# Performance work log

Measured on AMD Instinct MI355X. Metric: run time of the kernel, lower is better.

Reference implementation:

```python
import jax, jax.numpy as jnp
from jax import lax
import numpy as np

EVAL_TERMS = 10   # eval mode: num_terms = eval_terms, update_iters = 0
INIT_ITERS = 50   # power iterations done in __init__
KSIZE = 3
IDX = np.array([0, 1, 1, 2, 3, 4, 2, 4, 3])  # maps 5 coeffs -> 3x3 kernel
EPS = 1e-12


def _l2n(t, axis):
    return t / (jnp.sqrt(jnp.sum(t * t, axis=axis, keepdims=True)) + EPS)


def setup_inputs() -> dict:
    key = jax.random.key(0)
    kx, kw, kb, ku, kv = jax.random.split(key, 5)
    C = 64
    stdv = 1.0 / np.sqrt(C)
    return {
        "x": jax.random.normal(kx, (16, C, 192, 192), dtype=jnp.float32),
        "random_conv_filter": jax.random.normal(kw, (C, C, 5), dtype=jnp.float32) * stdv,
        "bias": jax.random.uniform(kb, (C,), dtype=jnp.float32, minval=-stdv, maxval=stdv),
        "u0": jax.random.normal(ku, (5, 1, C), dtype=jnp.float32),
        "v0": jax.random.normal(kv, (5, C, 1), dtype=jnp.float32),
    }


def _power_iter(A, u0, v0):
    # A: (num, C, C) (stop-gradient), u: (num,1,C), v: (num,C,1)
    u = _l2n(u0, 2)
    v = _l2n(v0, 1)
    def body(i, uv):
        u, v = uv
        v = _l2n(jnp.sum(A * u, axis=2, keepdims=True), 1)
        u = _l2n(jnp.sum(A * v, axis=1, keepdims=True), 2)
        return (u, v)
    return lax.fori_loop(0, INIT_ITERS, body, (u, v))


def reference(x, random_conv_filter, bias, u0, v0):
    C = random_conv_filter.shape[0]
    # skew-symmetric filter per coefficient slice: A = 0.5*(W - W^T)
    A = 0.5 * (random_conv_filter - jnp.transpose(random_conv_filter, (1, 0, 2)))
    A = jnp.transpose(A, (2, 0, 1))  # (num, C, C)
    # spectral norm via power iteration (buffers; no grad)
    u, v = _power_iter(lax.stop_gradient(A), u0, v0)
    u = lax.stop_gradient(u)
    v = lax.stop_gradient(v)
    sigmas = jnp.sum(A * v * u, axis=(1, 2))  # (num,), grad flows through A only
    An = A / sigmas[:, None, None]
    # Taylor series of expm: I + An + An^2/2! + ... (eval_terms=10)
    curr = An
    Fm = An
    for i in range(2, EVAL_TERMS + 1):
        curr = jnp.einsum('nij,njk->nik', curr, An) / float(i)
        Fm = Fm + curr
    Fm = Fm + jnp.eye(C, dtype=Fm.dtype)[None]
    Fm = jnp.transpose(Fm, (1, 2, 0))  # (C, C, num)
    # expand 5 coeffs to 3x3 kernel, then spatial ifft2 -> real
    K = Fm[:, :, IDX].reshape(C, C, KSIZE, KSIZE)
    K = jnp.fft.ifft2(K, axes=(-2, -1)).real.astype(x.dtype)
    w = x.shape[2]
    pad = w // KSIZE  # circular pad and matching dilation
    xp = jnp.pad(x, ((0, 0), (0, 0), (pad, pad), (pad, pad)), mode='wrap')
    z = lax.conv_general_dilated(
        xp, K, window_strides=(1, 1), padding='VALID',
        rhs_dilation=(pad, pad),
        dimension_numbers=('NCHW', 'OIHW', 'NCHW'))
    return z + bias[None, :, None, None]
```

## Files before the change

kernel.cpp:

```cpp
#include <hip/hip_runtime.h>

typedef __attribute__((ext_vector_type(8))) short short8;
typedef __attribute__((ext_vector_type(4))) float f32x4;
typedef __attribute__((ext_vector_type(4))) float float4v;
typedef __attribute__((ext_vector_type(4))) unsigned int u32x4;

__device__ __forceinline__ unsigned short f2bf(float f) {
    unsigned int u = __float_as_uint(f);
    u += 0x7fffu + ((u >> 16) & 1u);
    return (unsigned short)(u >> 16);
}

__device__ __forceinline__ float wavesum(float x) {
#pragma unroll
    for (int m = 1; m < 64; m <<= 1) x += __shfl_xor(x, m);
    return x;
}

__device__ __forceinline__ float wavemax(float x) {
#pragma unroll
    for (int m = 1; m < 64; m <<= 1) x = fmaxf(x, __shfl_xor(x, m));
    return x;
}

__device__ __forceinline__ float matvec64(const float* row, float y) {
    float ac[8] = {0.f, 0.f, 0.f, 0.f, 0.f, 0.f, 0.f, 0.f};
#pragma unroll
    for (int j = 0; j < 64; ++j) {
        const float yj =
            __uint_as_float(__builtin_amdgcn_readlane(__float_as_uint(y), j));
        ac[j & 7] = fmaf(row[j], yj, ac[j & 7]);
    }
    return ((ac[0] + ac[1]) + (ac[2] + ac[3])) + ((ac[4] + ac[5]) + (ac[6] + ac[7]));
}

__device__ __forceinline__ void gload16(const void* g, void* l) {
    __builtin_amdgcn_global_load_lds(
        (const __attribute__((address_space(1))) unsigned int*)g,
        (__attribute__((address_space(3))) unsigned int*)l, 16, 0, 0);
}

#define WTF_OFF       81920
#define WTOLD_OFF     745472
#define WS_NEEDED     1409024UL

#define FM_AFP   0
#define FM_R0    17408
#define FM_R1    34816
#define FM_SLOT  52224
#define FM_RED   76800
#define FM_SMEM  76928

__device__ __forceinline__ void fm_matmul_sb(char* sm, int srcOff, int bfSrcSlot,
                                             int dstOff, int bfDstSlot, int t) {
    const float* src = (const float*)(sm + srcOff);
    const unsigned short* bfS =
        (const unsigned short*)(sm + FM_SLOT) + bfSrcSlot * 4096;
    float* dst = (float*)(sm + dstOff);
    float* redf = (float*)(sm + FM_RED);
    const int lane = t & 63;
    const int wv = t >> 6;
    const int lm = lane & 15, lg = lane >> 4;
    f32x4 acc[4] = {};
    if (t < 256) {
#pragma unroll
        for (int kk = 0; kk < 2; ++kk) {
            const float* ap = src + (16 * wv + lm) * 68 + kk * 32 + lg * 8;
            const f32x4 a0 = *(const f32x4*)ap;
            const f32x4 a1 = *(const f32x4*)(ap + 4);
            short8 ah;
#pragma unroll
            for (int j = 0; j < 4; ++j) {
                ah[j] = (short)f2bf(a0[j]);
                ah[j + 4] = (short)f2bf(a1[j]);
            }
#pragma unroll
            for (int cf = 0; cf < 4; ++cf) {
                const short8 b =
                    *(const short8*)(bfS + ((kk * 4 + cf) * 64 + lane) * 8);
                acc[cf] = __builtin_amdgcn_mfma_f32_16x16x32_bf16(ah, b, acc[cf],
                                                                  0, 0, 0);
            }
        }
        float mx = 0.0f;
#pragma unroll
        for (int cf = 0; cf < 4; ++cf)
#pragma unroll
            for (int r = 0; r < 4; ++r) mx = fmaxf(mx, fabsf(acc[cf][r]));
        mx = wavemax(mx);
        if (lane == 0) redf[wv] = mx;
    }
    __syncthreads();
    if (t < 256) {
        const float g = fmaxf(fmaxf(redf[0], redf[1]), fmaxf(redf[2], redf[3]));
        const float sc = 1.0f / g;
        unsigned short* bfD = (unsigned short*)(sm + FM_SLOT) + bfDstSlot * 4096;
#pragma unroll
        for (int cf = 0; cf < 4; ++cf) {
#pragma unroll
            for (int r = 0; r < 4; ++r) {
                const int k = 16 * wv + 4 * lg + r;
                const int nn = 16 * cf + lm;
                const float v = acc[cf][r] * sc;
                dst[k * 68 + nn] = v;
                if (bfDstSlot >= 0)
                    bfD[(((k >> 5) * 4 + cf) * 64 + ((k & 31) >> 3) * 16 + lm) * 8 +
                        (k & 7)] = f2bf(v);
            }
        }
    }
    __syncthreads();
}

__global__ __launch_bounds__(512) void fm_kernel(const float* __restrict__ W,
                                                 const float* __restrict__ u0,
                                                 float* __restrict__ FmOut) {
    __shared__ __align__(16) char smem[FM_SMEM];
    const int t = threadIdx.x;
    float* Afp = (float*)(smem + FM_AFP);
    float* R0f = (float*)(smem + FM_R0);
    float* R1f = (float*)(smem + FM_R1);
    float* redf = (float*)(smem + FM_RED);
    float* sigP = redf + 4;
    const int n = blockIdx.x;
    const int lane = t & 63;
    const int wv = t >> 6;
    const int lm = lane & 15, lg = lane >> 4;

    {
        const int i = t >> 3;
        const int j0 = (t & 7) * 8;
#pragma unroll
        for (int k = 0; k < 8; ++k) {
            const int j = j0 + k;
            const float wij = W[(i * 64 + j) * 5 + n];
            const float wji = W[(j * 64 + i) * 5 + n];
            Afp[i * 68 + j] = 0.5f * (wij - wji);
        }
    }
    __syncthreads();

    if (t < 256) {
        unsigned short* s0 = (unsigned short*)(smem + FM_SLOT);
#pragma unroll
        for (int cf = 0; cf < 4; ++cf) {
#pragma unroll
            for (int r = 0; r < 4; ++r) {
                const int k = 16 * wv + 4 * lg + r;
                const int nn = 16 * cf + lm;
                s0[(((k >> 5) * 4 + cf) * 64 + ((k & 31) >> 3) * 16 + lm) * 8 +
                   (k & 7)] = f2bf(Afp[k * 68 + nn]);
            }
        }
    }
    __syncthreads();

    fm_matmul_sb(smem, FM_AFP, 0, FM_R0, 1, t);
    fm_matmul_sb(smem, FM_R0, 1, FM_R1, 2, t);
    fm_matmul_sb(smem, FM_R1, 2, FM_R0, 0, t);
    fm_matmul_sb(smem, FM_R0, 0, FM_R1, 2, t);
    fm_matmul_sb(smem, FM_R1, 2, FM_R0, 0, t);
    fm_matmul_sb(smem, FM_R0, 0, FM_R1, -1, t);
    fm_matmul_sb(smem, FM_R1, 0, FM_R0, -1, t);
    fm_matmul_sb(smem, FM_R0, 1, FM_R1, -1, t);

    if (t < 64) {
        float row[64];
#pragma unroll
        for (int q = 0; q < 16; ++q)
            *(f32x4*)&row[q * 4] = *(const f32x4*)&R1f[t * 68 + q * 4];
        float u = u0[n * 64 + t];
        u = u / (sqrtf(wavesum(u * u)) + 1e-12f);
        const float w = matvec64(row, u);
#pragma unroll
        for (int q = 0; q < 16; ++q)
            *(f32x4*)&row[q * 4] = *(const f32x4*)&Afp[t * 68 + q * 4];
        const float tt = matvec64(row, w);
        const float v = tt / (sqrtf(wavesum(tt * tt)) + 1e-12f);
        const float s = matvec64(row, v);
        const float u50 = -s / (sqrtf(wavesum(s * s)) + 1e-12f);
        const float t2 = matvec64(row, u50);
        const float sig = wavesum(v * t2);
        if (t == 0) *sigP = sig;
    }
    __syncthreads();

    const float inv_sig = 1.0f / (*sigP);
    float Fm[4][4];
    if (t < 256) {
        unsigned int* Anpk = (unsigned int*)(smem + FM_SLOT);
#pragma unroll
        for (int cf = 0; cf < 4; ++cf) {
#pragma unroll
            for (int r = 0; r < 4; ++r) {
                const int k = 16 * wv + 4 * lg + r;
                const int nn = 16 * cf + lm;
                const float v = Afp[k * 68 + nn] * inv_sig;
                R0f[k * 68 + nn] = v;
                const unsigned int ph = f2bf(v);
                const float hf = __uint_as_float(ph << 16);
                const unsigned int pl = f2bf(v - hf);
                Anpk[(((k >> 5) * 4 + cf) * 64 + ((k & 31) >> 3) * 16 + lm) * 8 +
                     (k & 7)] = ph | (pl << 16);
                Fm[cf][r] = v;
            }
        }
    }
    __syncthreads();

    for (int term = 2; term <= 10; ++term) {
        f32x4 acc[4] = {};
        if (t < 256) {
            const unsigned int* Anpk = (const unsigned int*)(smem + FM_SLOT);
#pragma unroll
            for (int kk = 0; kk < 2; ++kk) {
                const float* ap = R0f + (16 * wv + lm) * 68 + kk * 32 + lg * 8;
                const f32x4 a0 = *(const f32x4*)ap;
                const f32x4 a1 = *(const f32x4*)(ap + 4);
                short8 ah, al;
#pragma unroll
                for (int j = 0; j < 4; ++j) {
                    const unsigned int h0 = f2bf(a0[j]);
                    ah[j] = (short)h0;
                    al[j] = (short)f2bf(a0[j] - __uint_as_float(h0 << 16));
                    const unsigned int h1 = f2bf(a1[j]);
                    ah[j + 4] = (short)h1;
                    al[j + 4] = (short)f2bf(a1[j] - __uint_as_float(h1 << 16));
                }
#pragma unroll
                for (int cf = 0; cf < 4; ++cf) {
                    const unsigned int* pp = Anpk + ((kk * 4 + cf) * 64 + lane) * 8;
                    const u32x4 p0 = *(const u32x4*)pp;
                    const u32x4 p1 = *(const u32x4*)(pp + 4);
                    short8 bh, bl;
#pragma unroll
                    for (int j = 0; j < 4; ++j) {
                        bh[j] = (short)(p0[j] & 0xffffu);
                        bl[j] = (short)(p0[j] >> 16);
                        bh[j + 4] = (short)(p1[j] & 0xffffu);
                        bl[j + 4] = (short)(p1[j] >> 16);
                    }
                    acc[cf] = __builtin_amdgcn_mfma_f32_16x16x32_bf16(ah, bh,
                                                                      acc[cf], 0, 0, 0);
                    acc[cf] = __builtin_amdgcn_mfma_f32_16x16x32_bf16(ah, bl,
                                                                      acc[cf], 0, 0, 0);
                    acc[cf] = __builtin_amdgcn_mfma_f32_16x16x32_bf16(al, bh,
                                                                      acc[cf], 0, 0, 0);
                }
            }
        }
        __syncthreads();
        if (t < 256) {
            const float sc = 1.0f / (float)term;
#pragma unroll
            for (int cf = 0; cf < 4; ++cf) {
#pragma unroll
                for (int r = 0; r < 4; ++r) {
                    const int k = 16 * wv + 4 * lg + r;
                    const int nn = 16 * cf + lm;
                    const float v = acc[cf][r] * sc;
                    Fm[cf][r] += v;
                    if (term < 10) R0f[k * 68 + nn] = v;
                }
            }
        }
        __syncthreads();
    }

    if (t < 256) {
#pragma unroll
        for (int cf = 0; cf < 4; ++cf) {
#pragma unroll
            for (int r = 0; r < 4; ++r) {
                const int k = 16 * wv + 4 * lg + r;
                const int nn = 16 * cf + lm;
                FmOut[n * 4096 + k * 64 + nn] = Fm[cf][r] + ((k == nn) ? 1.0f : 0.0f);
            }
        }
    }
}

__global__ __launch_bounds__(256) void wbuild_kernel(const float* __restrict__ Fm,
                                                     unsigned short* __restrict__ Wtf,
                                                     unsigned short* __restrict__ WtOld) {
    const int tg = blockIdx.x * 256 + threadIdx.x;
    const int o = tg >> 6;
    const int i = tg & 63;
    float f[5];
#pragma unroll
    for (int nn = 0; nn < 5; ++nn) f[nn] = Fm[nn * 4096 + o * 64 + i];
    const int idx[3][3] = {{0, 1, 1}, {2, 3, 4}, {2, 4, 3}};
    float Kk[3][3];
#pragma unroll
    for (int u = 0; u < 3; ++u) {
#pragma unroll
        for (int v = 0; v < 3; ++v) {
            float s = 0.0f;
#pragma unroll
            for (int p = 0; p < 3; ++p) {
#pragma unroll
                for (int q = 0; q < 3; ++q) {
                    const int m = (p * u + q * v) % 3;
                    s += f[idx[p][q]] * ((m == 0) ? 1.0f : -0.5f);
                }
            }
            Kk[u][v] = s * (1.0f / 9.0f);
        }
    }
#pragma unroll
    for (int a = 0; a < 3; ++a) {
#pragma unroll
        for (int b = 0; b < 3; ++b) {
            const int m = (a * 3 + b) * 64 + o;
#pragma unroll
            for (int al = 0; al < 3; ++al) {
#pragma unroll
                for (int be = 0; be < 3; ++be) {
                    const int kh = (al - a + 4) % 3;
                    const int kw = (be - b + 4) % 3;
                    const unsigned short bf = f2bf(Kk[kh][kw]);
                    const int kap = (al * 3 + be) * 64 + i;
                    WtOld[m * 576 + kap] = bf;
                    const int MF = m >> 4, lmx = m & 15;
                    const int cc = kap >> 5, lgx = (kap >> 3) & 3, j = kap & 7;
                    Wtf[MF * 9216 + cc * 512 + (lgx * 16 + lmx) * 8 + j] = bf;
                }
            }
        }
    }
}

__global__ __launch_bounds__(256, 2) void gemm5_kernel(
    const float* __restrict__ x, const unsigned short* __restrict__ Wtf,
    const float* __restrict__ bias, float* __restrict__ out) {
    __shared__ __align__(16) char smem[81920];
    const int t = threadIdx.x;
    const int lane = t & 63;
    const int wv = t >> 6;
    const int wm = wv >> 1;
    const int wp = wv & 1;
    const int lm = lane & 15;
    const int lg = lane >> 4;

    const int orig = blockIdx.x;
    const int swz = (orig & 7) * 192 + (orig >> 3);
    const int mg = swz % 3;
    const int panel = swz / 3;
    const int n = panel >> 5;
    const int h0b = (panel & 31) * 2;

    const int sswz = (wv ^ ((lane >> 1) & 3)) * 16;
    const int rswz = (lg ^ ((lm >> 1) & 3)) * 16;

    f32x4 acc[6][4] = {};
    float R[4][8];

    const float* xb = x + (size_t)n * 2359296 + lane;

#define ASTAGE(BUF, KC)                                                         \
    {                                                                           \
        _Pragma("unroll") for (int it = 0; it < 6; ++it) {                      \
            char* ldsb = smem + (BUF) * 40960 + it * 4096 + wv * 1024;          \
            const int e = it * 2048 + t * 8;                                    \
            const int mfL = e >> 10;                                            \
            const int rem = e & 1023;                                           \
            gload16(Wtf + (mg * 12 + mfL) * 9216 + (KC) * 1024 + rem, ldsb);    \
        }                                                                       \
    }

#define BLOAD(KC)                                                               \
    {                                                                           \
        const int al_ = (KC) / 3, be_ = (KC) - 3 * ((KC) / 3);                  \
        const float* xc = xb + (h0b + 64 * al_) * 192 + be_ * 64;               \
        _Pragma("unroll") for (int j = 0; j < 4; ++j)                           \
            _Pragma("unroll") for (int k = 0; k < 8; ++k)                       \
                R[j][k] = xc[(size_t)((j >> 1) * 32 + wv * 8 + k) * 36864 +     \
                             (j & 1) * 192];                                    \
    }

#define BSTORE(BUF)                                                             \
    {                                                                           \
        _Pragma("unroll") for (int j = 0; j < 4; ++j) {                         \
            union { unsigned short us[8]; short8 v; } pk;                       \
            _Pragma("unroll") for (int k = 0; k < 8; ++k)                       \
                pk.us[k] = f2bf(R[j][k]);                                       \
            *(short8*)(smem + (BUF) * 40960 + 24576 + (j >> 1) * 8192 +         \
                       ((j & 1) * 64 + lane) * 64 + sswz) = pk.v;               \
        }                                                                       \
    }

#define COMPUTE(BUF)                                                            \
    {                                                                           \
        const char* base = smem + (BUF) * 40960;                                \
        short8 af[12];                                                          \
        short8 bf[8];                                                           \
        _Pragma("unroll") for (int mf = 0; mf < 6; ++mf)                        \
            _Pragma("unroll") for (int cl = 0; cl < 2; ++cl)                    \
                af[mf * 2 + cl] = *(const short8*)(                             \
                    base + (wm * 6 + mf) * 2048 + cl * 1024 + lane * 16);       \
        _Pragma("unroll") for (int pf = 0; pf < 4; ++pf)                        \
            _Pragma("unroll") for (int cl = 0; cl < 2; ++cl)                    \
                bf[pf * 2 + cl] = *(const short8*)(                             \
                    base + 24576 + cl * 8192 +                                  \
                    (wp * 64 + pf * 16 + lm) * 64 + rswz);                      \
        _Pragma("unroll") for (int cl = 0; cl < 2; ++cl)                        \
            _Pragma("unroll") for (int mf = 0; mf < 6; ++mf)                    \
                _Pragma("unroll") for (int pf = 0; pf < 4; ++pf)                \
                    acc[mf][pf] = __builtin_amdgcn_mfma_f32_16x16x32_bf16(      \
                        af[mf * 2 + cl], bf[pf * 2 + cl], acc[mf][pf], 0, 0, 0);\
    }

    BLOAD(0);
    ASTAGE(0, 0);
    BSTORE(0);
    __syncthreads();
#pragma unroll
    for (int kc = 0; kc < 9; ++kc) {
        const int b = kc & 1;
        if (kc < 8) {
            BLOAD(kc + 1);
            ASTAGE(b ^ 1, kc + 1);
        }
        COMPUTE(b);
        if (kc < 8) BSTORE(b ^ 1);
        __syncthreads();
    }
#undef ASTAGE
#undef BLOAD
#undef BSTORE
#undef COMPUTE

    const int h0 = h0b + wp;
#pragma unroll
    for (int mf = 0; mf < 6; ++mf) {
#pragma unroll
        for (int r = 0; r < 4; ++r) {
            const int m = mg * 192 + wm * 96 + mf * 16 + lg * 4 + r;
            const int o = m & 63;
            const int ab2 = m >> 6;
            const float bo = bias[o];
            const int rowoff =
                ((n * 64 + o) * 192 + (h0 + 64 * (ab2 / 3))) * 192 + 64 * (ab2 % 3);
#pragma unroll
            for (int pf = 0; pf < 4; ++pf) {
                out[rowoff + pf * 16 + lm] = acc[mf][pf][r] + bo;
            }
        }
    }
}

__global__ __launch_bounds__(256) void gemm_fallback(const float* __restrict__ x,
                                                     const unsigned short* __restrict__ Wt,
                                                     const float* __restrict__ bias,
                                                     float* __restrict__ out) {
    __shared__ unsigned short Xs[64][36];
    const int t = threadIdx.x;
    const int lane = t & 63;
    const int wv = t >> 6;
    const int pblk = blockIdx.x;
    const int mg = blockIdx.y;
    const int n = pblk >> 6;
    const int h0 = pblk & 63;
    const int wave_m0 = mg * 192 + wv * 48;
    const int lm = lane & 15;
    const int lg = lane >> 4;

    f32x4 acc[3][4] = {};
    const float* xb = x + n * 64 * 36864;
    const int w0s = t & 63;
    const int kq = (t >> 6) * 8;

    for (int c = 0; c < 18; ++c) {
        const int ab = c >> 1;
        const int al = ab / 3;
        const int be = ab % 3;
        const int ih = (c & 1) * 32;
        const int base = ih * 36864 + (h0 + 64 * al) * 192 + 64 * be + w0s;
#pragma unroll
        for (int s = 0; s < 8; ++s) {
            const int kp = kq + s;
            Xs[w0s][kp] = f2bf(xb[base + kp * 36864]);
        }
        __syncthreads();
        const int kb = c * 32 + lg * 8;
        short8 af[3];
#pragma unroll
        for (int mf = 0; mf < 3; ++mf)
            af[mf] = *(const short8*)(Wt + (wave_m0 + mf * 16 + lm) * 576 + kb);
        short8 bf[4];
#pragma unroll
        for (int pf = 0; pf < 4; ++pf) {
            union { short8 v; unsigned long long q[2]; } u;
            const unsigned long long* s8 =
                (const unsigned long long*)(&Xs[pf * 16 + lm][lg * 8]);
            u.q[0] = s8[0];
            u.q[1] = s8[1];
            bf[pf] = u.v;
        }
#pragma unroll
        for (int mf = 0; mf < 3; ++mf)
#pragma unroll
            for (int pf = 0; pf < 4; ++pf)
                acc[mf][pf] = __builtin_amdgcn_mfma_f32_16x16x32_bf16(
                    af[mf], bf[pf], acc[mf][pf], 0, 0, 0);
        __syncthreads();
    }

#pragma unroll
    for (int mf = 0; mf < 3; ++mf)
#pragma unroll
        for (int r = 0; r < 4; ++r) {
            const int m = wave_m0 + mf * 16 + lg * 4 + r;
            const int o = m & 63;
            const int ab2 = m >> 6;
            const float bo = bias[o];
            const int rowoff =
                ((n * 64 + o) * 192 + (h0 + 64 * (ab2 / 3))) * 192 + 64 * (ab2 % 3);
#pragma unroll
            for (int pf = 0; pf < 4; ++pf)
                out[rowoff + pf * 16 + lm] = acc[mf][pf][r] + bo;
        }
}

extern "C" void kernel_launch(void* const* d_in, const int* in_sizes, int n_in,
                              void* d_out, int out_size, void* d_ws, size_t ws_size,
                              hipStream_t stream) {
    (void)in_sizes; (void)n_in; (void)out_size;
    const float* x = (const float*)d_in[0];
    const float* W = (const float*)d_in[1];
    const float* bias = (const float*)d_in[2];
    const float* u0 = (const float*)d_in[3];
    float* out = (float*)d_out;

    float* Fm = (float*)d_ws;
    unsigned short* Wtf = (unsigned short*)((char*)d_ws + WTF_OFF);
    unsigned short* WtOld = (unsigned short*)((char*)d_ws + WTOLD_OFF);

    fm_kernel<<<5, 512, 0, stream>>>(W, u0, Fm);
    wbuild_kernel<<<16, 256, 0, stream>>>(Fm, Wtf, WtOld);

    if (ws_size >= WS_NEEDED) {
        gemm5_kernel<<<1536, 256, 0, stream>>>(x, Wtf, bias, out);
    } else {
        dim3 g(1024, 3, 1);
        gemm_fallback<<<g, 256, 0, stream>>>(x, WtOld, bias, out);
    }
}
```

Baseline: 128.3 us.

## Deepen GEMM prefetch to two stages and stage weights through registers

The main GEMM kernel now prefetches activation tiles two k-chunks ahead into alternating register sets instead of one. Weight tiles are no longer copied with direct global-to-LDS loads; they go into registers and are written to LDS after compute. The goal is to hide more global load latency behind the MFMA work. In exchange, register use rises a lot (a second 32-float buffer plus six 16-byte vectors), which may cause spills or lower occupancy under the 2-blocks launch bound.

```diff
diff --git a/kernel.cpp b/kernel.cpp
--- a/kernel.cpp
+++ b/kernel.cpp
@@ -32,12 +32,6 @@
         ac[j & 7] = fmaf(row[j], yj, ac[j & 7]);
     }
     return ((ac[0] + ac[1]) + (ac[2] + ac[3])) + ((ac[4] + ac[5]) + (ac[6] + ac[7]));
-}
-
-__device__ __forceinline__ void gload16(const void* g, void* l) {
-    __builtin_amdgcn_global_load_lds(
-        (const __attribute__((address_space(1))) unsigned int*)g,
-        (__attribute__((address_space(3))) unsigned int*)l, 16, 0, 0);
 }
 
 #define WTF_OFF       81920
@@ -330,7 +324,7 @@
     }
 }
 
-__global__ __launch_bounds__(256, 2) void gemm5_kernel(
+__global__ __launch_bounds__(256, 2) void gemm6_kernel(
     const float* __restrict__ x, const unsigned short* __restrict__ Wtf,
     const float* __restrict__ bias, float* __restrict__ out) {
     __shared__ __align__(16) char smem[81920];
@@ -353,40 +347,47 @@
     const int rswz = (lg ^ ((lm >> 1) & 3)) * 16;
 
     f32x4 acc[6][4] = {};
-    float R[4][8];
+    float RS0[4][8], RS1[4][8];
+    u32x4 WA[6];
 
     const float* xb = x + (size_t)n * 2359296 + lane;
 
-#define ASTAGE(BUF, KC)                                                         \
-    {                                                                           \
-        _Pragma("unroll") for (int it = 0; it < 6; ++it) {                      \
-            char* ldsb = smem + (BUF) * 40960 + it * 4096 + wv * 1024;          \
-            const int e = it * 2048 + t * 8;                                    \
-            const int mfL = e >> 10;                                            \
-            const int rem = e & 1023;                                           \
-            gload16(Wtf + (mg * 12 + mfL) * 9216 + (KC) * 1024 + rem, ldsb);    \
-        }                                                                       \
-    }
-
-#define BLOAD(KC)                                                               \
+#define BLOAD(KC, RS)                                                           \
     {                                                                           \
         const int al_ = (KC) / 3, be_ = (KC) - 3 * ((KC) / 3);                  \
         const float* xc = xb + (h0b + 64 * al_) * 192 + be_ * 64;               \
         _Pragma("unroll") for (int j = 0; j < 4; ++j)                           \
             _Pragma("unroll") for (int k = 0; k < 8; ++k)                       \
-                R[j][k] = xc[(size_t)((j >> 1) * 32 + wv * 8 + k) * 36864 +     \
-                             (j & 1) * 192];                                    \
-    }
-
-#define BSTORE(BUF)                                                             \
+                RS[j][k] = xc[(size_t)((j >> 1) * 32 + wv * 8 + k) * 36864 +    \
+                              (j & 1) * 192];                                   \
+    }
+
+#define BSTORE(BUF, RS)                                                         \
     {                                                                           \
         _Pragma("unroll") for (int j = 0; j < 4; ++j) {                         \
             union { unsigned short us[8]; short8 v; } pk;                       \
             _Pragma("unroll") for (int k = 0; k < 8; ++k)                       \
-                pk.us[k] = f2bf(R[j][k]);                                       \
+                pk.us[k] = f2bf(RS[j][k]);                                      \
             *(short8*)(smem + (BUF) * 40960 + 24576 + (j >> 1) * 8192 +         \
                        ((j & 1) * 64 + lane) * 64 + sswz) = pk.v;               \
         }                                                                       \
+    }
+
+#define ALOAD(KC)                                                               \
+    {                                                                           \
+        _Pragma("unroll") for (int it = 0; it < 6; ++it) {                      \
+            const int e = it * 2048 + t * 8;                                    \
+            const int mfL = e >> 10;                                            \
+            const int rem = e & 1023;                                           \
+            WA[it] = *(const u32x4*)(Wtf + (mg * 12 + mfL) * 9216 +             \
+                                     (KC) * 1024 + rem);                        \
+        }                                                                       \
+    }
+
+#define ASTORE(BUF)                                                             \
+    {                                                                           \
+        _Pragma("unroll") for (int it = 0; it < 6; ++it)                        \
+            *(u32x4*)(smem + (BUF) * 40960 + it * 4096 + t * 16) = WA[it];      \
     }
 
 #define COMPUTE(BUF)                                                            \
@@ -410,24 +411,32 @@
                         af[mf * 2 + cl], bf[pf * 2 + cl], acc[mf][pf], 0, 0, 0);\
     }
 
-    BLOAD(0);
-    ASTAGE(0, 0);
-    BSTORE(0);
-    __syncthreads();
+    BLOAD(0, RS0);
+    ALOAD(0);
+    BSTORE(0, RS0);
+    ASTORE(0);
+    ALOAD(1);
+    BLOAD(1, RS1);
+    __syncthreads();
+
 #pragma unroll
     for (int kc = 0; kc < 9; ++kc) {
         const int b = kc & 1;
+        if (kc < 7) {
+            if (b) { BLOAD(kc + 2, RS1); } else { BLOAD(kc + 2, RS0); }
+        }
+        COMPUTE(b);
         if (kc < 8) {
-            BLOAD(kc + 1);
-            ASTAGE(b ^ 1, kc + 1);
-        }
-        COMPUTE(b);
-        if (kc < 8) BSTORE(b ^ 1);
-        __syncthreads();
-    }
-#undef ASTAGE
+            if (b) { BSTORE(b ^ 1, RS0); } else { BSTORE(b ^ 1, RS1); }
+            ASTORE(b ^ 1);
+            if (kc < 7) ALOAD(kc + 2);
+            __syncthreads();
+        }
+    }
 #undef BLOAD
 #undef BSTORE
+#undef ALOAD
+#undef ASTORE
 #undef COMPUTE
 
     const int h0 = h0b + wp;
@@ -540,7 +549,7 @@
     wbuild_kernel<<<16, 256, 0, stream>>>(Fm, Wtf, WtOld);
 
     if (ws_size >= WS_NEEDED) {
-        gemm5_kernel<<<1536, 256, 0, stream>>>(x, Wtf, bias, out);
+        gemm6_kernel<<<1536, 256, 0, stream>>>(x, Wtf, bias, out);
     } else {
         dim3 g(1024, 3, 1);
         gemm_fallback<<<g, 256, 0, stream>>>(x, WtOld, bias, out);
```

After: 202.8 us. 58.0% more time.
